# Kernel optimization log

Measured on AMD Instinct MI355X. Metric: run time of the kernel, lower is better.

Reference implementation:

```python
import jax, jax.numpy as jnp
import numpy as np

B, S, D, H = 8, 2048, 256, 256


def setup_inputs() -> dict:
    key = jax.random.key(0)
    ks = jax.random.split(key, 7)
    s_ih = 1.0 / np.sqrt(D)
    s_hh = 1.0 / np.sqrt(H)
    return {
        "x": jax.random.normal(ks[0], (B, S, D), dtype=jnp.float32),
        "Wih_f": jax.random.uniform(ks[1], (4 * H, D), jnp.float32, -s_ih, s_ih),
        "bih_f": jax.random.uniform(ks[2], (4 * H,), jnp.float32, -s_ih, s_ih),
        "Whh_f": jax.random.uniform(ks[3], (4 * H, H), jnp.float32, -s_hh, s_hh),
        "Wih_b": jax.random.uniform(ks[4], (4 * H, D), jnp.float32, -s_ih, s_ih),
        "bih_b": jax.random.uniform(ks[5], (4 * H,), jnp.float32, -s_ih, s_ih),
        "Whh_b": jax.random.uniform(ks[6], (4 * H, H), jnp.float32, -s_hh, s_hh),
    }


def _lstm_dir(x, Wih, bih, Whh, reverse):
    # Precompute input projection for all timesteps in one GEMM: [B,S,4H]
    b, s, _ = x.shape
    h_dim = Whh.shape[1]
    x_proj = jnp.einsum("bsd,gd->bsg", x, Wih) + bih

    def step(carry, xt):  # xt: [B,4H]
        h, c = carry
        gates = xt + h @ Whh.T
        i, f, g, o = jnp.split(gates, 4, axis=-1)
        i = jax.nn.sigmoid(i)
        f = jax.nn.sigmoid(f)
        o = jax.nn.sigmoid(o)
        g = jnp.tanh(g)
        c = f * c + i * g
        h = o * jnp.tanh(c)
        return (h, c), h

    init = (jnp.zeros((b, h_dim), x.dtype), jnp.zeros((b, h_dim), x.dtype))
    # scan over time; reverse=True processes t=S-1..0 and stacks outputs in
    # original time order, matching the torch backward loop with insert(0, .)
    _, hs = jax.lax.scan(step, init, jnp.swapaxes(x_proj, 0, 1), reverse=reverse)
    return jnp.swapaxes(hs, 0, 1)  # [B,S,H]


def reference(x, Wih_f, bih_f, Whh_f, Wih_b, bih_b, Whh_b):
    fwd = _lstm_dir(x, Wih_f, bih_f, Whh_f, reverse=False)
    bwd = _lstm_dir(x, Wih_b, bih_b, Whh_b, reverse=True)
    return jnp.concatenate([fwd, bwd], axis=-1)  # [B,S,2H]
```

## Files before the change

### kernel.cpp

```cpp
#include <hip/hip_runtime.h>
#include <hip/hip_bf16.h>
#include <stdint.h>

#define SQ   2048
#define NB   8
#define G4   1024
#define NROW 16384

typedef float f32x4 __attribute__((ext_vector_type(4)));
typedef short bf16x8 __attribute__((ext_vector_type(8)));
typedef uint32_t u32;
typedef unsigned long long u64;

__device__ __forceinline__ f32x4 mfma16(bf16x8 a, bf16x8 b, f32x4 c) {
  return __builtin_amdgcn_mfma_f32_16x16x32_bf16(a, b, c, 0, 0, 0);
}
__device__ __forceinline__ u32 pk_bf16(float lo, float hi) {
  u32 r;
  asm("v_cvt_pk_bf16_f32 %0, %1, %2" : "=v"(r) : "v"(lo), "v"(hi));
  return r;
}
__device__ __forceinline__ float bf_lo(u32 u){ union{u32 a; float f;} x; x.a = u << 16;        return x.f; }
__device__ __forceinline__ float bf_hi(u32 u){ union{u32 a; float f;} x; x.a = u & 0xffff0000u; return x.f; }

__device__ __forceinline__ float sigm(float x)   { return 1.0f / (1.0f + __expf(-x)); }
__device__ __forceinline__ float tanh_f(float x) { return 1.0f - 2.0f / (__expf(2.0f * x) + 1.0f); }

#define PINA(x) asm volatile("" : "+a"(x))

__device__ __forceinline__ u64 ld_fast(const u64* p) {
  u64 v;
  asm volatile("global_load_dwordx2 %0, %1, off sc0\n\ts_waitcnt vmcnt(0)"
               : "=v"(v) : "v"(p) : "memory");
  return v;
}
__device__ __forceinline__ void st_fast(u64* p, u64 v) {
  asm volatile("global_store_dwordx2 %0, %1, off sc0" :: "v"(p), "v"(v) : "memory");
}

__global__ __launch_bounds__(256) void xproj_gemm(
    const float* __restrict__ x,
    const float* __restrict__ WihF, const float* __restrict__ bihF,
    const float* __restrict__ WihB, const float* __restrict__ bihB,
    uint16_t* __restrict__ xp)
{
  const int dir = blockIdx.z;
  const float* Wih = dir ? WihB : WihF;
  const float* bih = dir ? bihB : bihF;
  char* xpd = (char*)xp + (size_t)dir * ((size_t)NROW * G4 * 2);

  const int g0 = blockIdx.y * 128;
  const int m0 = blockIdx.x * 128;

  __shared__ union {
    struct { short A[128 * 72]; short B[128 * 72]; } s;
    short T[128 * 136];
  } u;
  __shared__ float biasS[128];

  const int tid  = threadIdx.x;
  const int lane = tid & 63;
  const int w    = tid >> 6;
  const int wg   = w >> 1;
  const int wm   = w & 1;
  const int l15  = lane & 15;
  const int l4   = lane >> 4;

  if (tid < 128) biasS[tid] = bih[g0 + tid];

  f32x4 acc[4][4] = {};

  const int r_st = tid >> 1;
  const int half = tid & 1;
  const int mrow_st = m0 + r_st;
  const int xb = mrow_st & 7;
  const int xt = mrow_st >> 3;
  const float* xrow = x + ((size_t)xb * SQ + xt) * 256;
  const float* wrow = Wih + (size_t)(g0 + r_st) * 256;

  for (int s = 0; s < 4; ++s) {
    const int k0 = s * 64;
    __syncthreads();
    {
      const float* srcA = wrow + k0 + half * 32;
      const float* srcB = xrow + k0 + half * 32;
      short* dstA = u.s.A + r_st * 72 + half * 32;
      short* dstB = u.s.B + r_st * 72 + half * 32;
      #pragma unroll
      for (int j = 0; j < 4; ++j) {
        f32x4 a0 = *(const f32x4*)(srcA + j * 8);
        f32x4 a1 = *(const f32x4*)(srcA + j * 8 + 4);
        uint4 pa = { pk_bf16(a0.x, a0.y), pk_bf16(a0.z, a0.w),
                     pk_bf16(a1.x, a1.y), pk_bf16(a1.z, a1.w) };
        *(uint4*)(dstA + j * 8) = pa;
        f32x4 b0 = *(const f32x4*)(srcB + j * 8);
        f32x4 b1 = *(const f32x4*)(srcB + j * 8 + 4);
        uint4 pb = { pk_bf16(b0.x, b0.y), pk_bf16(b0.z, b0.w),
                     pk_bf16(b1.x, b1.y), pk_bf16(b1.z, b1.w) };
        *(uint4*)(dstB + j * 8) = pb;
      }
    }
    __syncthreads();
    #pragma unroll
    for (int kt = 0; kt < 2; ++kt) {
      bf16x8 aF[4], bF[4];
      #pragma unroll
      for (int i = 0; i < 4; ++i) {
        const int ar = wg * 64 + i * 16 + l15;
        const int br = wm * 64 + i * 16 + l15;
        aF[i] = *(const bf16x8*)(u.s.A + ar * 72 + kt * 32 + l4 * 8);
        bF[i] = *(const bf16x8*)(u.s.B + br * 72 + kt * 32 + l4 * 8);
      }
      #pragma unroll
      for (int i = 0; i < 4; ++i)
        #pragma unroll
        for (int j = 0; j < 4; ++j)
          acc[i][j] = mfma16(aF[i], bF[j], acc[i][j]);
    }
  }

  __syncthreads();
  #pragma unroll
  for (int i = 0; i < 4; ++i) {
    const f32x4 bv = *(const f32x4*)(biasS + wg * 64 + i * 16 + l4 * 4);
    #pragma unroll
    for (int j = 0; j < 4; ++j) {
      f32x4 v = acc[i][j];
      v.x += bv.x; v.y += bv.y; v.z += bv.z; v.w += bv.w;
      const int mrow = wm * 64 + j * 16 + l15;
      const int gcol = wg * 64 + i * 16 + l4 * 4;
      uint2 p; p.x = pk_bf16(v.x, v.y); p.y = pk_bf16(v.z, v.w);
      *(uint2*)(u.T + mrow * 136 + gcol) = p;
    }
  }
  __syncthreads();
  {
    const char* trow = (const char*)(u.T + r_st * 136);
    char* orow = xpd + (size_t)(m0 + r_st) * 2048 + g0 * 2;
    #pragma unroll
    for (int j = 0; j < 8; ++j) {
      const int local = half * 128 + j * 16;
      uint4 v = *(const uint4*)(trow + local);
      *(uint4*)(orow + local) = v;
    }
  }
}

__global__ __launch_bounds__(256, 1) void lstm_rec(
    const float* __restrict__ WhhF, const float* __restrict__ WhhB,
    const uint16_t* __restrict__ xp, float* __restrict__ out,
    u64* exs, u64* exf)
{
  __shared__ alignas(16) uint16_t hF[2][8][264];

  const int bid = blockIdx.x;
  const int dir = bid & 7;
  const int c   = bid >> 3;
  if (dir > 1) return;

  const float* Whh = dir ? WhhB : WhhF;
  const uint16_t* xpd = xp + (size_t)dir * NROW * G4;

  const int tid  = threadIdx.x;
  const int lane = tid & 63;
  const int w    = tid >> 6;
  const int l15  = lane & 15;
  const int l4   = lane >> 4;
  const int bcl  = lane & 7;
  const int qsel = (lane >> 3) & 1;

  bf16x8 W[4][8];
  #pragma unroll
  for (int g = 0; g < 4; ++g) {
    const int row = g * 256 + c * 64 + w * 16 + l15;
    const float* src = Whh + (size_t)row * 256 + l4 * 8;
    #pragma unroll
    for (int kt = 0; kt < 8; ++kt) {
      f32x4 v0 = *(const f32x4*)(src + kt * 32);
      f32x4 v1 = *(const f32x4*)(src + kt * 32 + 4);
      union { bf16x8 v; u32 u[4]; } pk;
      pk.u[0] = pk_bf16(v0.x, v0.y); pk.u[1] = pk_bf16(v0.z, v0.w);
      pk.u[2] = pk_bf16(v1.x, v1.y); pk.u[3] = pk_bf16(v1.z, v1.w);
      W[g][kt] = pk.v;
      PINA(W[g][kt]);
    }
  }

  u64* exf_me = exf + (size_t)(dir * 4 + c) * 512;
  u64* exs_me = exs + (size_t)(dir * 4 + c) * 512;
  const u64* pf[3]; const u64* ps[3];
  #pragma unroll
  for (int j = 0; j < 3; ++j) {
    const int cc = (c + 1 + j) & 3;
    pf[j] = exf + (size_t)(dir * 4 + cc) * 512;
    ps[j] = exs + (size_t)(dir * 4 + cc) * 512;
  }
  const int cc0 = ((c + 1) & 3) * 64, cc1 = ((c + 2) & 3) * 64, cc2 = ((c + 3) & 3) * 64;
  const int sb = tid >> 5, sp2 = (tid & 31) * 2;

  const int d0   = w * 16 + l4 * 4 + qsel * 2;
  const int word = bcl * 32 + (d0 >> 1);
  float c0 = 0.0f, c1 = 0.0f;

  u32 xq[4], xqn[4];
  {
    const int tt0 = dir ? SQ - 1 : 0;
    const uint16_t* xr = xpd + (size_t)(tt0 * 8 + bcl) * 1024 + c * 64 + d0;
    #pragma unroll
    for (int g = 0; g < 4; ++g) xq[g] = *(const u32*)(xr + g * 256);
  }

  int slowMode = 0, slowWins = 0;

  #pragma unroll 1
  for (int t = 0; t < SQ; ++t) {
    const int tt = dir ? (SQ - 1 - t) : t;

    if (t > 0) {
      const u32 want = (u32)t;
      const size_t soff = (size_t)((t - 1) & 1) * 256 + tid;
      u64 pw0, pw1, pw2;
      if (!slowMode) {
        asm volatile(
          "global_load_dwordx2 %0, %3, off sc0\n\t"
          "global_load_dwordx2 %1, %4, off sc0\n\t"
          "global_load_dwordx2 %2, %5, off sc0\n\t"
          "s_waitcnt vmcnt(0)"
          : "=v"(pw0), "=v"(pw1), "=v"(pw2)
          : "v"(pf[0] + soff), "v"(pf[1] + soff), "v"(pf[2] + soff)
          : "memory");
      } else {
        pw0 = __hip_atomic_load(ps[0] + soff, __ATOMIC_RELAXED, __HIP_MEMORY_SCOPE_AGENT);
        pw1 = __hip_atomic_load(ps[1] + soff, __ATOMIC_RELAXED, __HIP_MEMORY_SCOPE_AGENT);
        pw2 = __hip_atomic_load(ps[2] + soff, __ATOMIC_RELAXED, __HIP_MEMORY_SCOPE_AGENT);
      }
      int anySlow = 0;
      #pragma unroll
      for (int j = 0; j < 3; ++j) {
        u64& pw = (j == 0) ? pw0 : (j == 1) ? pw1 : pw2;
        int tries = 0;
        while ((u32)pw != want) {
          ++tries;
          if (slowMode || tries > 8) {
            anySlow = 1;
            pw = __hip_atomic_load(ps[j] + soff, __ATOMIC_RELAXED,
                                   __HIP_MEMORY_SCOPE_AGENT);
          } else {
            pw = ld_fast(pf[j] + soff);
          }
        }
      }
      if (!slowMode && anySlow) { if (++slowWins >= 4) slowMode = 1; }

      uint16_t* hrow = &hF[(t - 1) & 1][sb][0];
      *(u32*)(hrow + cc0 + sp2) = (u32)(pw0 >> 32);
      *(u32*)(hrow + cc1 + sp2) = (u32)(pw1 >> 32);
      *(u32*)(hrow + cc2 + sp2) = (u32)(pw2 >> 32);
    }
    asm volatile("s_waitcnt lgkmcnt(0)" ::: "memory");
    __builtin_amdgcn_s_barrier();

    {
      const int tn = (t + 1 < SQ) ? t + 1 : SQ - 1;
      const int ttn = dir ? (SQ - 1 - tn) : tn;
      const uint16_t* xr = xpd + (size_t)(ttn * 8 + bcl) * 1024 + c * 64 + d0;
      #pragma unroll
      for (int g = 0; g < 4; ++g) xqn[g] = *(const u32*)(xr + g * 256);
    }

    f32x4 acc[4] = {};
    if (t > 0) {
      #pragma unroll
      for (int kt = 0; kt < 8; ++kt) {
        const bf16x8 bF = *(const bf16x8*)&hF[(t - 1) & 1][bcl][kt * 32 + l4 * 8];
        #pragma unroll
        for (int g = 0; g < 4; ++g) acc[g] = mfma16(W[g][kt], bF, acc[g]);
      }
    }

    float P0[4], P1[4];
    #pragma unroll
    for (int g = 0; g < 4; ++g) {
      P0[g] = (qsel ? acc[g].z : acc[g].x) + bf_lo(xq[g]);
      P1[g] = (qsel ? acc[g].w : acc[g].y) + bf_hi(xq[g]);
    }
    const float i0 = sigm(P0[0]), f0 = sigm(P0[1]), g0v = tanh_f(P0[2]), o0 = sigm(P0[3]);
    const float i1 = sigm(P1[0]), f1 = sigm(P1[1]), g1v = tanh_f(P1[2]), o1 = sigm(P1[3]);
    c0 = f0 * c0 + i0 * g0v;
    c1 = f1 * c1 + i1 * g1v;
    const float h0 = o0 * tanh_f(c0);
    const float h1 = o1 * tanh_f(c1);

    const u32 h01 = pk_bf16(h0, h1);
    const u64 pub = ((u64)h01 << 32) | (u64)(u32)(t + 1);
    st_fast(exf_me + (size_t)(t & 1) * 256 + word, pub);
    __hip_atomic_store(exs_me + (size_t)(t & 1) * 256 + word, pub,
                       __ATOMIC_RELAXED, __HIP_MEMORY_SCOPE_AGENT);
    *(u32*)&hF[t & 1][bcl][c * 64 + d0] = h01;
    *(float2*)(out + ((size_t)bcl * SQ + tt) * 512 + dir * 256 + c * 64 + d0) =
        make_float2(h0, h1);

    #pragma unroll
    for (int g = 0; g < 4; ++g) xq[g] = xqn[g];
  }
}

extern "C" void kernel_launch(void* const* d_in, const int* in_sizes, int n_in,
                              void* d_out, int out_size, void* d_ws, size_t ws_size,
                              hipStream_t stream) {
  const float* x    = (const float*)d_in[0];
  const float* WihF = (const float*)d_in[1];
  const float* bihF = (const float*)d_in[2];
  const float* WhhF = (const float*)d_in[3];
  const float* WihB = (const float*)d_in[4];
  const float* bihB = (const float*)d_in[5];
  const float* WhhB = (const float*)d_in[6];
  float* out = (float*)d_out;

  const size_t XPB = (size_t)2 * NROW * G4 * 2;
  const size_t EXB = (size_t)4096 * sizeof(u64);
  if (ws_size < XPB + 2 * EXB) return;
  uint16_t* xpw = (uint16_t*)d_ws;
  u64* exs = (u64*)((char*)d_ws + XPB);
  u64* exf = (u64*)((char*)d_ws + XPB + EXB);

  hipMemsetAsync(exs, 0, 2 * EXB, stream);
  xproj_gemm<<<dim3(128, 8, 2), dim3(256), 0, stream>>>(x, WihF, bihF, WihB, bihB, xpw);
  lstm_rec<<<dim3(32), dim3(256), 0, stream>>>(WhhF, WhhB, xpw, out, exs, exf);
}
```

Baseline: 6.057 ms.

## Move recurrent weights from registers into swizzled LDS and prefetch half per step

The recurrent Whh slice, previously held as bf16 fragments pinned in AGPRs, is now staged once into 128KB of dynamic shared memory with an XOR swizzle. Each timestep reads the fragments back from LDS: the first half of K is prefetched before the inter-block exchange wait and the second half is loaded inline next to the MFMAs. This frees a large register budget and tries to hide LDS latency behind the exchange wait, but it adds LDS traffic on the serial recurrence critical path.

```diff
diff --git a/kernel.cpp b/kernel.cpp
--- a/kernel.cpp
+++ b/kernel.cpp
@@ -25,8 +25,6 @@
 
 __device__ __forceinline__ float sigm(float x)   { return 1.0f / (1.0f + __expf(-x)); }
 __device__ __forceinline__ float tanh_f(float x) { return 1.0f - 2.0f / (__expf(2.0f * x) + 1.0f); }
-
-#define PINA(x) asm volatile("" : "+a"(x))
 
 __device__ __forceinline__ u64 ld_fast(const u64* p) {
   u64 v;
@@ -151,7 +149,9 @@
     const uint16_t* __restrict__ xp, float* __restrict__ out,
     u64* exs, u64* exf)
 {
-  __shared__ alignas(16) uint16_t hF[2][8][264];
+  extern __shared__ char smem[];
+  uint16_t* Wl = (uint16_t*)smem;
+  uint16_t (*hF)[8][264] = (uint16_t (*)[8][264])(smem + 131072);
 
   const int bid = blockIdx.x;
   const int dir = bid & 7;
@@ -169,20 +169,19 @@
   const int bcl  = lane & 7;
   const int qsel = (lane >> 3) & 1;
 
-  bf16x8 W[4][8];
-  #pragma unroll
-  for (int g = 0; g < 4; ++g) {
-    const int row = g * 256 + c * 64 + w * 16 + l15;
-    const float* src = Whh + (size_t)row * 256 + l4 * 8;
-    #pragma unroll
-    for (int kt = 0; kt < 8; ++kt) {
-      f32x4 v0 = *(const f32x4*)(src + kt * 32);
-      f32x4 v1 = *(const f32x4*)(src + kt * 32 + 4);
-      union { bf16x8 v; u32 u[4]; } pk;
-      pk.u[0] = pk_bf16(v0.x, v0.y); pk.u[1] = pk_bf16(v0.z, v0.w);
-      pk.u[2] = pk_bf16(v1.x, v1.y); pk.u[3] = pk_bf16(v1.z, v1.w);
-      W[g][kt] = pk.v;
-      PINA(W[g][kt]);
+  {
+    const int r = tid;
+    const int g = r >> 6, rr = r & 63;
+    const float* src = Whh + (size_t)(g * 256 + c * 64 + rr) * 256;
+    char* drow = (char*)Wl + r * 512;
+    const int sw = (r & 7) << 4;
+    #pragma unroll 4
+    for (int ch = 0; ch < 32; ++ch) {
+      f32x4 v0 = *(const f32x4*)(src + ch * 8);
+      f32x4 v1 = *(const f32x4*)(src + ch * 8 + 4);
+      uint4 p = { pk_bf16(v0.x, v0.y), pk_bf16(v0.z, v0.w),
+                  pk_bf16(v1.x, v1.y), pk_bf16(v1.z, v1.w) };
+      *(uint4*)(drow + ((ch * 16) ^ sw)) = p;
     }
   }
 
@@ -202,6 +201,12 @@
   const int word = bcl * 32 + (d0 >> 1);
   float c0 = 0.0f, c1 = 0.0f;
 
+  const int swr = (l15 & 7) << 4;
+  const char* arow[4];
+  #pragma unroll
+  for (int g = 0; g < 4; ++g)
+    arow[g] = (const char*)Wl + (g * 64 + w * 16 + l15) * 512;
+
   u32 xq[4], xqn[4];
   {
     const int tt0 = dir ? SQ - 1 : 0;
@@ -211,10 +216,18 @@
   }
 
   int slowMode = 0, slowWins = 0;
+  __syncthreads();
 
   #pragma unroll 1
   for (int t = 0; t < SQ; ++t) {
     const int tt = dir ? (SQ - 1 - t) : t;
+
+    bf16x8 aPre[4][4];
+    #pragma unroll
+    for (int kt = 0; kt < 4; ++kt)
+      #pragma unroll
+      for (int g = 0; g < 4; ++g)
+        aPre[kt][g] = *(const bf16x8*)(arow[g] + ((kt * 64 + l4 * 16) ^ swr));
 
     if (t > 0) {
       const u32 want = (u32)t;
@@ -270,11 +283,21 @@
 
     f32x4 acc[4] = {};
     if (t > 0) {
-      #pragma unroll
-      for (int kt = 0; kt < 8; ++kt) {
-        const bf16x8 bF = *(const bf16x8*)&hF[(t - 1) & 1][bcl][kt * 32 + l4 * 8];
+      const uint16_t* hrow = &hF[(t - 1) & 1][bcl][0];
+      #pragma unroll
+      for (int kt = 0; kt < 4; ++kt) {
+        const bf16x8 bF = *(const bf16x8*)(hrow + kt * 32 + l4 * 8);
         #pragma unroll
-        for (int g = 0; g < 4; ++g) acc[g] = mfma16(W[g][kt], bF, acc[g]);
+        for (int g = 0; g < 4; ++g) acc[g] = mfma16(aPre[kt][g], bF, acc[g]);
+      }
+      #pragma unroll
+      for (int kt = 4; kt < 8; ++kt) {
+        const bf16x8 bF = *(const bf16x8*)(hrow + kt * 32 + l4 * 8);
+        #pragma unroll
+        for (int g = 0; g < 4; ++g) {
+          const bf16x8 aF = *(const bf16x8*)(arow[g] + ((kt * 64 + l4 * 16) ^ swr));
+          acc[g] = mfma16(aF, bF, acc[g]);
+        }
       }
     }
 
@@ -324,7 +347,11 @@
   u64* exs = (u64*)((char*)d_ws + XPB);
   u64* exf = (u64*)((char*)d_ws + XPB + EXB);
 
+  const int LDSZ = 131072 + 2 * 8 * 264 * 2;
+  (void)hipFuncSetAttribute((const void*)lstm_rec,
+                            hipFuncAttributeMaxDynamicSharedMemorySize, LDSZ);
+
   hipMemsetAsync(exs, 0, 2 * EXB, stream);
   xproj_gemm<<<dim3(128, 8, 2), dim3(256), 0, stream>>>(x, WihF, bihF, WihB, bihB, xpw);
-  lstm_rec<<<dim3(32), dim3(256), 0, stream>>>(WhhF, WhhB, xpw, out, exs, exf);
-}
+  lstm_rec<<<dim3(32), dim3(256), LDSZ, stream>>>(WhhF, WhhB, xpw, out, exs, exf);
+}
```

Result: slower. 6.344 ms (+4.7%).
